# Kernel optimization log

Measured on AMD Instinct MI355X. Metric: run time of the kernel, lower is better.

The kernel has to match this reference:

```python
import jax, jax.numpy as jnp
import numpy as np
from functools import partial

T, B, IN, H, OUT = 512, 64, 512, 1024, 512


def _qrnn_layer(x, W, b):
    """One QRNN layer (window=1, fo-pool). x: (T,B,D) -> (T,B,H)."""
    g = jnp.einsum('tbd,dh->tbh', x, W) + b        # (T,B,3H)
    z, f, o = jnp.split(g, 3, axis=-1)
    z = jnp.tanh(z)
    f = jax.nn.sigmoid(f)
    o = jax.nn.sigmoid(o)

    def step(c, zf):
        z_t, f_t = zf
        c = f_t * c + (1.0 - f_t) * z_t            # fo-pool recurrence
        return c, c

    c0 = jnp.zeros((x.shape[1], W.shape[1] // 3), x.dtype)
    _, cs = jax.lax.scan(step, c0, (z, f))         # cs: (T,B,H)
    return o * cs


def setup_inputs() -> dict:
    key = jax.random.key(0)
    ks = jax.random.split(key, 5)
    scale = lambda fan_in: 1.0 / np.sqrt(fan_in)
    return {
        'x':   jax.random.normal(ks[0], (T, B, IN), jnp.float32),
        'W0':  jax.random.normal(ks[1], (IN, 3 * H), jnp.float32) * scale(IN),
        'b0':  jnp.zeros((3 * H,), jnp.float32),
        'W1':  jax.random.normal(ks[2], (H, 3 * H), jnp.float32) * scale(H),
        'b1':  jnp.zeros((3 * H,), jnp.float32),
        'Wfc': jax.random.normal(ks[3], (H, OUT), jnp.float32) * scale(H),
        'bfc': jnp.zeros((OUT,), jnp.float32),
    }


def reference(x, W0, b0, W1, b1, Wfc, bfc):
    h = _qrnn_layer(x, W0, b0)                     # layer 0: (T,B,H)
    h = _qrnn_layer(h, W1, b1)                     # layer 1: (T,B,H)
    out = jnp.einsum('tbh,ho->tbo', h, Wfc) + bfc  # fc over all timesteps
    return out
```

## Files before the change

kernel.cpp:

```cpp
#include <hip/hip_runtime.h>
#include <hip/hip_bf16.h>


#define QT 512
#define QB 64
#define QIN 512
#define QH 1024
#define QOUT 512
#define QM (QT * QB)
#define SEG 32
#define SL (QT / SEG)

typedef unsigned short ushort_t;
typedef __attribute__((ext_vector_type(8))) short bf16x8;
typedef __attribute__((ext_vector_type(4))) float f32x4;

__device__ __forceinline__ float u2f(ushort_t u) {
    union { unsigned int i; float f; } v;
    v.i = ((unsigned int)u) << 16;
    return v.f;
}

__device__ __forceinline__ ushort_t f2bf(float f) {
    union { float f; unsigned int i; } v;
    v.f = f;
    unsigned int r = v.i + 0x7fffu + ((v.i >> 16) & 1u);
    return (ushort_t)(r >> 16);
}

__device__ __forceinline__ void glds16(const ushort_t* g, ushort_t* l) {
    __builtin_amdgcn_global_load_lds(
        (const __attribute__((address_space(1))) void*)g,
        (__attribute__((address_space(3))) void*)l, 16, 0, 0);
}

__global__ __launch_bounds__(256) void cvt_bf16(const float* __restrict__ src,
                                                ushort_t* __restrict__ dst) {
    const int i = blockIdx.x * 256 + threadIdx.x;
    float4 v = ((const float4*)src)[i];
    ushort4 o;
    o.x = f2bf(v.x); o.y = f2bf(v.y); o.z = f2bf(v.z); o.w = f2bf(v.w);
    ((ushort4*)dst)[i] = o;
}

__global__ __launch_bounds__(256) void transpose_cvt(
    const float* __restrict__ W, ushort_t* __restrict__ WT, int K, int N) {
    __shared__ float t[32][33];
    const int tx = threadIdx.x & 31, ty = threadIdx.x >> 5;
    const int n0 = blockIdx.x * 32, k0 = blockIdx.y * 32;
#pragma unroll
    for (int i = 0; i < 4; ++i)
        t[ty + 8 * i][tx] = W[(size_t)(k0 + ty + 8 * i) * N + n0 + tx];
    __syncthreads();
#pragma unroll
    for (int i = 0; i < 4; ++i)
        WT[(size_t)(n0 + ty + 8 * i) * K + k0 + tx] = f2bf(t[tx][ty + 8 * i]);
}

template <int MODE, int K>
__global__ __launch_bounds__(512, 2) void gemm256(
    const ushort_t* __restrict__ A, const ushort_t* __restrict__ BT,
    const float* __restrict__ bias, void* __restrict__ out,
    int c0, int CW) {
    constexpr int NT = K / 32;
    __shared__ ushort_t As[4 * 8192];
    __shared__ ushort_t Bs[4 * 8192];

    const int tid = threadIdx.x;
    const int lane = tid & 63;
    const int w = tid >> 6;
    const int wr = w >> 2, wc = w & 3;

    const int gx = gridDim.x;
    const int nwg = gx * gridDim.y;
    int flat = blockIdx.y * gx + blockIdx.x;
    flat = (flat & 7) * (nwg >> 3) + (flat >> 3);
    const int by = flat / gx;
    const int bx = flat - by * gx;
    const int m0 = by * 256;

    int nW, nOut, outstride, gate = 0;
    if (MODE == 0) {
        const int per = CW >> 8;
        gate = bx / per;
        const int nloc = (bx - gate * per) * 256;
        nW = gate * QH + c0 + nloc;
        nOut = gate * CW + nloc;
        outstride = 3 * CW;
    } else {
        nW = bx * 256;
        nOut = nW;
        outstride = QOUT;
    }

    size_t aoff[2], boff[2];
    int ldso[2];
#pragma unroll
    for (int j = 0; j < 2; ++j) {
        const int c = w * 128 + j * 64 + lane;
        const int r = c >> 2;
        const int gs = (c & 3) ^ ((r >> 1) & 3);
        aoff[j] = (size_t)(m0 + r) * K + gs * 8;
        boff[j] = (size_t)(nW + r) * K + gs * 8;
        ldso[j] = w * 1024 + j * 512;
    }

    const int fl = lane & 15, fq = lane >> 4;
    const int laneoff = fl * 32 + ((fq ^ ((fl >> 1) & 3)) << 3);

    f32x4 acc[8][4];
#pragma unroll
    for (int i = 0; i < 8; ++i)
#pragma unroll
        for (int j = 0; j < 4; ++j) acc[i][j] = {0.f, 0.f, 0.f, 0.f};

#pragma unroll
    for (int t = 0; t < 3; ++t) {
        const int slot = t * 8192;
#pragma unroll
        for (int j = 0; j < 2; ++j)
            glds16(A + aoff[j] + t * 32, &As[slot + ldso[j]]);
#pragma unroll
        for (int j = 0; j < 2; ++j)
            glds16(BT + boff[j] + t * 32, &Bs[slot + ldso[j]]);
    }
    asm volatile("s_waitcnt vmcnt(8)" ::: "memory");
    __builtin_amdgcn_s_barrier();

    for (int kt = 0; kt < NT; ++kt) {
        const int slot = (kt & 3) * 8192;
        const int sa = slot + wr * 4096 + laneoff;
        const int sb = slot + wc * 2048 + laneoff;
        const bool pf = (kt + 3 < NT);
        const int pslot = ((kt + 3) & 3) * 8192;
        const size_t kb = (size_t)(kt + 3) * 32;

        bf16x8 a0[4], a1[4], bv[4];
#pragma unroll
        for (int i = 0; i < 4; ++i) a0[i] = *(const bf16x8*)&As[sa + i * 512];
#pragma unroll
        for (int j = 0; j < 4; ++j) bv[j] = *(const bf16x8*)&Bs[sb + j * 512];
        if (pf) {
#pragma unroll
            for (int j = 0; j < 2; ++j)
                glds16(A + aoff[j] + kb, &As[pslot + ldso[j]]);
        }
        __builtin_amdgcn_sched_barrier(0);
        __builtin_amdgcn_s_barrier();
        asm volatile("s_waitcnt lgkmcnt(0)" ::: "memory");
        __builtin_amdgcn_sched_barrier(0);
        __builtin_amdgcn_s_setprio(1);
#pragma unroll
        for (int i = 0; i < 4; ++i)
#pragma unroll
            for (int j = 0; j < 4; ++j)
                acc[i][j] = __builtin_amdgcn_mfma_f32_16x16x32_bf16(
                    a0[i], bv[j], acc[i][j], 0, 0, 0);
        __builtin_amdgcn_s_setprio(0);
        __builtin_amdgcn_sched_barrier(0);
        __builtin_amdgcn_s_barrier();
#pragma unroll
        for (int i = 0; i < 4; ++i)
            a1[i] = *(const bf16x8*)&As[sa + (4 + i) * 512];
        if (pf) {
#pragma unroll
            for (int j = 0; j < 2; ++j)
                glds16(BT + boff[j] + kb, &Bs[pslot + ldso[j]]);
        }
        __builtin_amdgcn_sched_barrier(0);
        __builtin_amdgcn_s_barrier();
        asm volatile("s_waitcnt lgkmcnt(0)" ::: "memory");
        __builtin_amdgcn_sched_barrier(0);
        __builtin_amdgcn_s_setprio(1);
#pragma unroll
        for (int i = 0; i < 4; ++i)
#pragma unroll
            for (int j = 0; j < 4; ++j)
                acc[4 + i][j] = __builtin_amdgcn_mfma_f32_16x16x32_bf16(
                    a1[i], bv[j], acc[4 + i][j], 0, 0, 0);
        __builtin_amdgcn_s_setprio(0);
        if (kt < NT - 3)
            asm volatile("s_waitcnt vmcnt(8)" ::: "memory");
        else if (kt == NT - 3)
            asm volatile("s_waitcnt vmcnt(4)" ::: "memory");
        else if (kt == NT - 2)
            asm volatile("s_waitcnt vmcnt(0)" ::: "memory");
        __builtin_amdgcn_sched_barrier(0);
        if (kt < NT - 1) __builtin_amdgcn_s_barrier();
    }

    const float ak = (gate == 0) ? 2.8853900817779268f : -1.4426950408889634f;
    const float aa = (gate == 0) ? -2.f : 1.f;
    const float ad = (gate == 0) ? 1.f : 0.f;

    float bvv[4];
#pragma unroll
    for (int j = 0; j < 4; ++j) bvv[j] = bias[nW + wc * 64 + j * 16 + fl];
#pragma unroll
    for (int i = 0; i < 8; ++i) {
#pragma unroll
        for (int r = 0; r < 4; ++r) {
            const int row = m0 + wr * 128 + i * 16 + fq * 4 + r;
#pragma unroll
            for (int j = 0; j < 4; ++j) {
                const int col = nOut + wc * 64 + j * 16 + fl;
                float v = acc[i][j][r] + bvv[j];
                if (MODE == 0) {
                    v = aa * __builtin_amdgcn_rcpf(
                                 1.f + __builtin_amdgcn_exp2f(ak * v)) +
                        ad;
                    ((ushort_t*)out)[(size_t)row * outstride + col] = f2bf(v);
                } else {
                    ((float*)out)[(size_t)row * outstride + col] = v;
                }
            }
        }
    }
}


__global__ __launch_bounds__(256) void scan_p1(const ushort_t* __restrict__ g,
                                               float* __restrict__ Aseg,
                                               float* __restrict__ Bseg,
                                               int CW) {
    const int idx = blockIdx.x * 256 + threadIdx.x;
    const int hh = idx % CW;
    const int sb = idx / CW;
    const int b = sb % QB;
    const int s = sb / QB;
    const ushort_t* gp = g + ((size_t)(s * SL * QB + b) * 3) * CW + hh;
    const size_t grow = (size_t)QB * 3 * CW;
    float zv[SL], fv[SL];
#pragma unroll
    for (int t = 0; t < SL; ++t) {
        zv[t] = u2f(gp[0]);
        fv[t] = u2f(gp[CW]);
        gp += grow;
    }
    float A = 1.f, Bc = 0.f;
#pragma unroll
    for (int t = 0; t < SL; ++t) {
        Bc = fv[t] * Bc + (1.f - fv[t]) * zv[t];
        A *= fv[t];
    }
    Aseg[idx] = A;
    Bseg[idx] = Bc;
}

__global__ __launch_bounds__(256) void scan_p2(const float* __restrict__ Aseg,
                                               const float* __restrict__ Bseg,
                                               float* __restrict__ cstart,
                                               int CW) {
    const int idx = blockIdx.x * 256 + threadIdx.x;
    const size_t stride = (size_t)QB * CW;
    float Av[SEG], Bv[SEG];
#pragma unroll
    for (int s = 0; s < SEG; ++s) {
        Av[s] = Aseg[s * stride + idx];
        Bv[s] = Bseg[s * stride + idx];
    }
    float c = 0.f;
#pragma unroll
    for (int s = 0; s < SEG; ++s) {
        cstart[s * stride + idx] = c;
        c = Av[s] * c + Bv[s];
    }
}

__global__ __launch_bounds__(256) void scan_p3(const ushort_t* __restrict__ g,
                                               const float* __restrict__ cstart,
                                               ushort_t* __restrict__ h,
                                               int c0, int CW) {
    const int idx = blockIdx.x * 256 + threadIdx.x;
    const int hh = idx % CW;
    const int sb = idx / CW;
    const int b = sb % QB;
    const int s = sb / QB;
    const ushort_t* gp = g + ((size_t)(s * SL * QB + b) * 3) * CW + hh;
    ushort_t* hp = h + (size_t)(s * SL * QB + b) * QH + c0 + hh;
    const size_t grow = (size_t)QB * 3 * CW;
    const size_t hrow = (size_t)QB * QH;
    float zv[SL], fv[SL], ov[SL];
#pragma unroll
    for (int t = 0; t < SL; ++t) {
        zv[t] = u2f(gp[0]);
        fv[t] = u2f(gp[CW]);
        ov[t] = u2f(gp[2 * CW]);
        gp += grow;
    }
    float c = cstart[idx];
#pragma unroll
    for (int t = 0; t < SL; ++t) {
        c = fv[t] * c + (1.f - fv[t]) * zv[t];
        *hp = f2bf(ov[t] * c);
        hp += hrow;
    }
}

extern "C" void kernel_launch(void* const* d_in, const int* in_sizes, int n_in,
                              void* d_out, int out_size, void* d_ws,
                              size_t ws_size, hipStream_t stream) {
    const float* x   = (const float*)d_in[0];
    const float* W0  = (const float*)d_in[1];
    const float* b0  = (const float*)d_in[2];
    const float* W1  = (const float*)d_in[3];
    const float* b1  = (const float*)d_in[4];
    const float* Wfc = (const float*)d_in[5];
    const float* bfc = (const float*)d_in[6];
    float* out = (float*)d_out;

    char* p = (char*)d_ws;
    ushort_t* h0   = (ushort_t*)p;  p += (size_t)QM * QH * 2;
    ushort_t* h1   = (ushort_t*)p;
    ushort_t* x_bf = (ushort_t*)p;  p += (size_t)QM * QH * 2;
    ushort_t* W0T  = (ushort_t*)p;  p += (size_t)3 * QH * QIN * 2;
    ushort_t* W1T  = (ushort_t*)p;  p += (size_t)3 * QH * QH * 2;
    ushort_t* WfcT = (ushort_t*)p;  p += (size_t)QOUT * QH * 2;
    const size_t base = (size_t)(p - (char*)d_ws);

    int CW = QH;
    while (CW > 256 &&
           base + 3 * (size_t)QB * CW * SEG * 4 + (size_t)QM * 3 * CW * 2 >
               ws_size)
        CW >>= 1;
    const int nch = QH / CW;

    float* Aseg   = (float*)p;  p += (size_t)QB * CW * SEG * 4;
    float* Bseg   = (float*)p;  p += (size_t)QB * CW * SEG * 4;
    float* cstart = (float*)p;  p += (size_t)QB * CW * SEG * 4;
    ushort_t* g   = (ushort_t*)p;

    dim3 blk(256);
    dim3 blk5(512);

    cvt_bf16<<<dim3(QM * QIN / 1024), blk, 0, stream>>>(x, x_bf);
    transpose_cvt<<<dim3(3 * QH / 32, QIN / 32), blk, 0, stream>>>(
        W0, W0T, QIN, 3 * QH);
    transpose_cvt<<<dim3(3 * QH / 32, QH / 32), blk, 0, stream>>>(
        W1, W1T, QH, 3 * QH);
    transpose_cvt<<<dim3(QOUT / 32, QH / 32), blk, 0, stream>>>(
        Wfc, WfcT, QH, QOUT);

    const dim3 ggrid(3 * (CW >> 8), QM / 256);
    const dim3 p13grid(SEG * QB * CW / 256);
    const dim3 p2grid(QB * CW / 256);

    for (int ci = 0; ci < nch; ++ci) {
        gemm256<0, QIN><<<ggrid, blk5, 0, stream>>>(x_bf, W0T, b0, g,
                                                    ci * CW, CW);
        scan_p1<<<p13grid, blk, 0, stream>>>(g, Aseg, Bseg, CW);
        scan_p2<<<p2grid, blk, 0, stream>>>(Aseg, Bseg, cstart, CW);
        scan_p3<<<p13grid, blk, 0, stream>>>(g, cstart, h0, ci * CW, CW);
    }
    for (int ci = 0; ci < nch; ++ci) {
        gemm256<0, QH><<<ggrid, blk5, 0, stream>>>(h0, W1T, b1, g,
                                                   ci * CW, CW);
        scan_p1<<<p13grid, blk, 0, stream>>>(g, Aseg, Bseg, CW);
        scan_p2<<<p2grid, blk, 0, stream>>>(Aseg, Bseg, cstart, CW);
        scan_p3<<<p13grid, blk, 0, stream>>>(g, cstart, h1, ci * CW, CW);
    }
    gemm256<1, QH><<<dim3(QOUT / 256, QM / 256), blk5, 0, stream>>>(
        h1, WfcT, bfc, out, 0, 0);
}
```

Baseline: 674.8 us.

## Vectorize scan kernels to four channels per thread and fold segment-prefix pass into scan_p3

Each scan thread now processes four adjacent hidden channels using 8-byte bf16 loads and float4 stores instead of one channel with 2-byte loads. The separate scan_p2 kernel that computed per-segment start states is removed. Instead, scan_p3 recomputes the carry-in by serially combining all preceding segment (A,B) pairs, which removes a launch and a global round trip for cstart. The trade-off is redundant prefix work that grows with segment index, plus four times fewer threads and higher register pressure from the 4-wide arrays.

```diff
diff --git a/kernel.cpp b/kernel.cpp
--- a/kernel.cpp
+++ b/kernel.cpp
@@ -18,6 +18,18 @@
 __device__ __forceinline__ float u2f(ushort_t u) {
     union { unsigned int i; float f; } v;
     v.i = ((unsigned int)u) << 16;
+    return v.f;
+}
+
+__device__ __forceinline__ float blo(unsigned int u) {
+    union { unsigned int i; float f; } v;
+    v.i = u << 16;
+    return v.f;
+}
+
+__device__ __forceinline__ float bhi(unsigned int u) {
+    union { unsigned int i; float f; } v;
+    v.i = u & 0xffff0000u;
     return v.f;
 }
 
@@ -223,76 +235,85 @@
                                                float* __restrict__ Aseg,
                                                float* __restrict__ Bseg,
                                                int CW) {
-    const int idx = blockIdx.x * 256 + threadIdx.x;
-    const int hh = idx % CW;
-    const int sb = idx / CW;
+    const int idx4 = blockIdx.x * 256 + threadIdx.x;
+    const int cw4 = CW >> 2;
+    const int hh = (idx4 % cw4) << 2;
+    const int sb = idx4 / cw4;
     const int b = sb % QB;
     const int s = sb / QB;
     const ushort_t* gp = g + ((size_t)(s * SL * QB + b) * 3) * CW + hh;
     const size_t grow = (size_t)QB * 3 * CW;
-    float zv[SL], fv[SL];
+    uint2 zu[SL], fu[SL];
 #pragma unroll
     for (int t = 0; t < SL; ++t) {
-        zv[t] = u2f(gp[0]);
-        fv[t] = u2f(gp[CW]);
+        zu[t] = *(const uint2*)gp;
+        fu[t] = *(const uint2*)(gp + CW);
         gp += grow;
     }
-    float A = 1.f, Bc = 0.f;
+    float4 A = {1.f, 1.f, 1.f, 1.f}, Bc = {0.f, 0.f, 0.f, 0.f};
 #pragma unroll
     for (int t = 0; t < SL; ++t) {
-        Bc = fv[t] * Bc + (1.f - fv[t]) * zv[t];
-        A *= fv[t];
-    }
-    Aseg[idx] = A;
-    Bseg[idx] = Bc;
-}
-
-__global__ __launch_bounds__(256) void scan_p2(const float* __restrict__ Aseg,
+        const float f0 = blo(fu[t].x), f1 = bhi(fu[t].x);
+        const float f2 = blo(fu[t].y), f3 = bhi(fu[t].y);
+        Bc.x = f0 * Bc.x + (1.f - f0) * blo(zu[t].x);
+        Bc.y = f1 * Bc.y + (1.f - f1) * bhi(zu[t].x);
+        Bc.z = f2 * Bc.z + (1.f - f2) * blo(zu[t].y);
+        Bc.w = f3 * Bc.w + (1.f - f3) * bhi(zu[t].y);
+        A.x *= f0; A.y *= f1; A.z *= f2; A.w *= f3;
+    }
+    const size_t oidx = (size_t)sb * CW + hh;
+    *(float4*)&Aseg[oidx] = A;
+    *(float4*)&Bseg[oidx] = Bc;
+}
+
+__global__ __launch_bounds__(256) void scan_p3(const ushort_t* __restrict__ g,
+                                               const float* __restrict__ Aseg,
                                                const float* __restrict__ Bseg,
-                                               float* __restrict__ cstart,
-                                               int CW) {
-    const int idx = blockIdx.x * 256 + threadIdx.x;
-    const size_t stride = (size_t)QB * CW;
-    float Av[SEG], Bv[SEG];
-#pragma unroll
-    for (int s = 0; s < SEG; ++s) {
-        Av[s] = Aseg[s * stride + idx];
-        Bv[s] = Bseg[s * stride + idx];
-    }
-    float c = 0.f;
-#pragma unroll
-    for (int s = 0; s < SEG; ++s) {
-        cstart[s * stride + idx] = c;
-        c = Av[s] * c + Bv[s];
-    }
-}
-
-__global__ __launch_bounds__(256) void scan_p3(const ushort_t* __restrict__ g,
-                                               const float* __restrict__ cstart,
                                                ushort_t* __restrict__ h,
                                                int c0, int CW) {
-    const int idx = blockIdx.x * 256 + threadIdx.x;
-    const int hh = idx % CW;
-    const int sb = idx / CW;
+    const int idx4 = blockIdx.x * 256 + threadIdx.x;
+    const int cw4 = CW >> 2;
+    const int hh = (idx4 % cw4) << 2;
+    const int sb = idx4 / cw4;
     const int b = sb % QB;
     const int s = sb / QB;
     const ushort_t* gp = g + ((size_t)(s * SL * QB + b) * 3) * CW + hh;
     ushort_t* hp = h + (size_t)(s * SL * QB + b) * QH + c0 + hh;
     const size_t grow = (size_t)QB * 3 * CW;
     const size_t hrow = (size_t)QB * QH;
-    float zv[SL], fv[SL], ov[SL];
+    uint2 zu[SL], fu[SL], ou[SL];
 #pragma unroll
     for (int t = 0; t < SL; ++t) {
-        zv[t] = u2f(gp[0]);
-        fv[t] = u2f(gp[CW]);
-        ov[t] = u2f(gp[2 * CW]);
+        zu[t] = *(const uint2*)gp;
+        fu[t] = *(const uint2*)(gp + CW);
+        ou[t] = *(const uint2*)(gp + 2 * CW);
         gp += grow;
     }
-    float c = cstart[idx];
+    float4 c = {0.f, 0.f, 0.f, 0.f};
+    const size_t stride = (size_t)QB * CW;
+    const size_t colo = (size_t)b * CW + hh;
+    for (int sp = 0; sp < s; ++sp) {
+        const float4 Av = *(const float4*)&Aseg[sp * stride + colo];
+        const float4 Bv = *(const float4*)&Bseg[sp * stride + colo];
+        c.x = Av.x * c.x + Bv.x;
+        c.y = Av.y * c.y + Bv.y;
+        c.z = Av.z * c.z + Bv.z;
+        c.w = Av.w * c.w + Bv.w;
+    }
 #pragma unroll
     for (int t = 0; t < SL; ++t) {
-        c = fv[t] * c + (1.f - fv[t]) * zv[t];
-        *hp = f2bf(ov[t] * c);
+        const float f0 = blo(fu[t].x), f1 = bhi(fu[t].x);
+        const float f2 = blo(fu[t].y), f3 = bhi(fu[t].y);
+        c.x = f0 * c.x + (1.f - f0) * blo(zu[t].x);
+        c.y = f1 * c.y + (1.f - f1) * bhi(zu[t].x);
+        c.z = f2 * c.z + (1.f - f2) * blo(zu[t].y);
+        c.w = f3 * c.w + (1.f - f3) * bhi(zu[t].y);
+        ushort4 hv;
+        hv.x = f2bf(blo(ou[t].x) * c.x);
+        hv.y = f2bf(bhi(ou[t].x) * c.y);
+        hv.z = f2bf(blo(ou[t].y) * c.z);
+        hv.w = f2bf(bhi(ou[t].y) * c.w);
+        *(ushort4*)hp = hv;
         hp += hrow;
     }
 }
@@ -327,7 +348,7 @@
 
     float* Aseg   = (float*)p;  p += (size_t)QB * CW * SEG * 4;
     float* Bseg   = (float*)p;  p += (size_t)QB * CW * SEG * 4;
-    float* cstart = (float*)p;  p += (size_t)QB * CW * SEG * 4;
+    p += (size_t)QB * CW * SEG * 4;
     ushort_t* g   = (ushort_t*)p;
 
     dim3 blk(256);
@@ -342,22 +363,19 @@
         Wfc, WfcT, QH, QOUT);
 
     const dim3 ggrid(3 * (CW >> 8), QM / 256);
-    const dim3 p13grid(SEG * QB * CW / 256);
-    const dim3 p2grid(QB * CW / 256);
+    const dim3 p13grid(SEG * QB * CW / 1024);
 
     for (int ci = 0; ci < nch; ++ci) {
         gemm256<0, QIN><<<ggrid, blk5, 0, stream>>>(x_bf, W0T, b0, g,
                                                     ci * CW, CW);
         scan_p1<<<p13grid, blk, 0, stream>>>(g, Aseg, Bseg, CW);
-        scan_p2<<<p2grid, blk, 0, stream>>>(Aseg, Bseg, cstart, CW);
-        scan_p3<<<p13grid, blk, 0, stream>>>(g, cstart, h0, ci * CW, CW);
+        scan_p3<<<p13grid, blk, 0, stream>>>(g, Aseg, Bseg, h0, ci * CW, CW);
     }
     for (int ci = 0; ci < nch; ++ci) {
         gemm256<0, QH><<<ggrid, blk5, 0, stream>>>(h0, W1T, b1, g,
                                                    ci * CW, CW);
         scan_p1<<<p13grid, blk, 0, stream>>>(g, Aseg, Bseg, CW);
-        scan_p2<<<p2grid, blk, 0, stream>>>(Aseg, Bseg, cstart, CW);
-        scan_p3<<<p13grid, blk, 0, stream>>>(g, cstart, h1, ci * CW, CW);
+        scan_p3<<<p13grid, blk, 0, stream>>>(g, Aseg, Bseg, h1, ci * CW, CW);
     }
     gemm256<1, QH><<<dim3(QOUT / 256, QM / 256), blk5, 0, stream>>>(
         h1, WfcT, bfc, out, 0, 0);
```

Result: no change. 669.6 us (-0.8%).
